# Kernel tuning notes

Hardware: AMD Instinct MI355X
Metric: run time of the kernel (lower is better)

## Reference

```python
import jax, jax.numpy as jnp
import numpy as np

B, N, D, K = 16, 1024, 512, 32
EPS = 1e-12  # F.normalize default eps


def setup_inputs() -> dict:
    key = jax.random.key(0)
    k1, k2, k3 = jax.random.split(key, 3)
    x = jax.random.normal(k1, (B, N, D), dtype=jnp.float32)
    mask = (jax.random.uniform(k2, (B, N)) < 0.9).astype(jnp.float32)
    centroids = jax.random.uniform(k3, (D, K), dtype=jnp.float32)
    # _init_params: conv.weight = 2*alpha*centroids, conv.bias = -alpha*||centroids||_col
    W = 2.0 * centroids
    b = -jnp.linalg.norm(centroids, axis=0)
    return {"x": x, "mask": mask, "W": W, "b": b, "centroids": centroids}


def reference(x, mask, W, b, centroids):
    # descriptor-wise L2 normalization (normalize_input=True)
    xn = x / jnp.maximum(jnp.linalg.norm(x, axis=2, keepdims=True), EPS)
    # 1x1 conv (matmul) + bias, masked logits
    logits = (jnp.einsum('bnd,dk->bnk', xn, W) + b) * mask[:, :, None]
    soft_assign = jax.nn.softmax(logits, axis=2) * mask[:, :, None]  # (B,N,K)
    # entropy with -log2(0) -> 0 (matches log_p[isinf]=0 since sa*0 = 0 there)
    safe = jnp.where(soft_assign > 0, soft_assign, 1.0)
    assign_entropy = -(soft_assign * jnp.log2(safe)).sum() / mask.sum()
    # cluster-usage distribution
    assign_sum = soft_assign.sum(axis=1)  # (B,K)
    assign_dist = jax.nn.log_softmax(assign_sum, axis=1)
    # NetVLAD residual pooling, algebraically fused (avoids (B,N,D,K) tensor):
    # vlad[b,d,k] = sum_n xn*sa - centroids[d,k]*sum_n sa
    vlad = jnp.einsum('bnd,bnk->bdk', xn, soft_assign) - centroids[None] * assign_sum[:, None, :]
    vlad = vlad / jnp.maximum(jnp.linalg.norm(vlad, axis=1, keepdims=True), EPS)
    vlad = jnp.transpose(vlad, (0, 2, 1))  # (B,K,D)
    return (vlad, assign_dist, assign_entropy)
```

## Files before the change

kernel.cpp:

```cpp
#include <hip/hip_runtime.h>
#include <math.h>

#define B 16
#define N 1024
#define D 512
#define K 32
#define EPSF 1e-12f

#define WS_CT_F   0
#define WS_ASP_F  16384
#define WS_ENTP_F 49152
#define WS_MSKP_F 50176
#define WS_PART_F 51200

#define OFF_DIST 262144
#define OFF_ENT  262656

typedef __attribute__((ext_vector_type(8))) short s16x8;
typedef __attribute__((ext_vector_type(4))) short s16x4;
typedef __attribute__((ext_vector_type(4))) float f32x4;

__device__ __forceinline__ ushort f2b(float f) {
    unsigned u = __builtin_bit_cast(unsigned, f);
    u += 0x7fffu + ((u >> 16) & 1u);
    return (ushort)(u >> 16);
}
__device__ __forceinline__ float b2f(ushort u) {
    return __builtin_bit_cast(float, (unsigned)u << 16);
}

struct SH {
    union U {
        ushort wtl[32 * 512];
        struct Q {
            ushort xs[4 * 2048];
            ushort xsT[512 * 36];
        } q;
    } u;
    ushort tls[32 * 32];
    float4 accsh[2 * 128];
    float ssqsh[32], invsh[32];
};

__global__ __launch_bounds__(256, 2) void kA2(const float* __restrict__ x,
    const float* __restrict__ mask, const float* __restrict__ Wf,
    const float* __restrict__ bias, const float* __restrict__ cent,
    float* __restrict__ ws, ushort* __restrict__ parts)
{
    __shared__ SH sh;
    const int bid = blockIdx.x;
    const int b = bid >> 4;
    const int s64 = bid & 15;
    const int tid = threadIdx.x;
    const int w = tid >> 6;
    const int rw = w & 1, dw = w >> 1;
    const int l = tid & 63;
    const int g = l >> 4, lo = l & 15;

    if (tid < 64) {
        int k = tid & 31, dd = tid >> 5;
        int d = bid * 2 + dd;
        ws[WS_CT_F + k * 512 + d] = cent[d * 32 + k];
    }
    {
        const float4* Wg = (const float4*)Wf;
        #pragma unroll
        for (int i = 0; i < 16; ++i) {
            int f4 = tid + i * 256;
            float4 v = Wg[f4];
            int d = f4 >> 3, k4 = (f4 & 7) << 2;
            float vv[4] = {v.x, v.y, v.z, v.w};
            #pragma unroll
            for (int j = 0; j < 4; ++j) {
                int k = k4 + j;
                sh.u.wtl[(k * 512 + d) ^ ((k & 7) << 3)] = f2b(vv[j]);
            }
        }
    }
    __syncthreads();
    s16x8 afr0[2][4], afr1[2][4];
    #pragma unroll
    for (int cc = 0; cc < 2; ++cc)
        #pragma unroll
        for (int ks = 0; ks < 4; ++ks) {
            int dglob = (dw * 2 + cc) * 128 + ks * 32 + g * 8;
            afr0[cc][ks] = *(const s16x8*)&sh.u.wtl[(lo * 512 + dglob) ^ ((lo & 7) << 3)];
            afr1[cc][ks] = *(const s16x8*)&sh.u.wtl[((16 + lo) * 512 + dglob) ^ ((lo & 7) << 3)];
        }
    __syncthreads();

    ushort* xw = sh.u.q.xs + w * 2048;
    ushort* xsT = sh.u.q.xsT;

    f32x4 acc2[2][8];
    #pragma unroll
    for (int kt = 0; kt < 2; ++kt)
        #pragma unroll
        for (int dt = 0; dt < 8; ++dt)
            acc2[kt][dt] = (f32x4){0.f, 0.f, 0.f, 0.f};

    #pragma unroll
    for (int tile = 0; tile < 2; ++tile) {
        const int n0 = s64 * 64 + tile * 32 + rw * 16;
        const int p = bid * 4 + tile * 2 + rw;

        float ssq[8] = {0.f, 0.f, 0.f, 0.f, 0.f, 0.f, 0.f, 0.f};
        f32x4 acc[2] = {{0.f, 0.f, 0.f, 0.f}, {0.f, 0.f, 0.f, 0.f}};
        const float4* xg = (const float4*)(x + (size_t)(b * N + n0) * D);

        #pragma unroll
        for (int cc = 0; cc < 2; ++cc) {
            const int c = dw * 2 + cc;
            float4 fv[8];
            #pragma unroll
            for (int j = 0; j < 8; ++j) {
                int idx = l + 64 * j;
                fv[j] = xg[(idx >> 5) * 128 + c * 32 + (idx & 31)];
            }
            #pragma unroll
            for (int j = 0; j < 8; ++j)
                ssq[j] += fv[j].x * fv[j].x + fv[j].y * fv[j].y
                        + fv[j].z * fv[j].z + fv[j].w * fv[j].w;
            #pragma unroll
            for (int j = 0; j < 8; ++j) {
                int idx = l + 64 * j;
                int r = idx >> 5, c4 = idx & 31;
                unsigned bo = (unsigned)(c4 * 8) ^ (unsigned)((r & 7) << 4);
                s16x4 sv = { (short)f2b(fv[j].x), (short)f2b(fv[j].y),
                             (short)f2b(fv[j].z), (short)f2b(fv[j].w) };
                *(s16x4*)&xw[r * 128 + (bo >> 1)] = sv;
                int nn = rw * 16 + r;
                int dbase = c * 128 + c4 * 4;
                xsT[(dbase + 0) * 36 + nn] = (ushort)sv[0];
                xsT[(dbase + 1) * 36 + nn] = (ushort)sv[1];
                xsT[(dbase + 2) * 36 + nn] = (ushort)sv[2];
                xsT[(dbase + 3) * 36 + nn] = (ushort)sv[3];
            }
            #pragma unroll
            for (int ks = 0; ks < 4; ++ks) {
                unsigned bo = (unsigned)(ks * 64 + g * 16) ^ (unsigned)((lo & 7) << 4);
                s16x8 bfrag = *(const s16x8*)&xw[lo * 128 + (bo >> 1)];
                acc[0] = __builtin_amdgcn_mfma_f32_16x16x32_bf16(afr0[cc][ks], bfrag, acc[0], 0, 0, 0);
                acc[1] = __builtin_amdgcn_mfma_f32_16x16x32_bf16(afr1[cc][ks], bfrag, acc[1], 0, 0, 0);
            }
        }

        #pragma unroll
        for (int j = 0; j < 8; ++j) {
            #pragma unroll
            for (int m = 16; m; m >>= 1) ssq[j] += __shfl_xor(ssq[j], m);
        }
        if (dw == 1) {
            if ((l & 31) == 0) {
                #pragma unroll
                for (int j = 0; j < 8; ++j)
                    sh.ssqsh[rw * 16 + (l >> 5) + 2 * j] = ssq[j];
            }
            sh.accsh[rw * 128 + l * 2 + 0] = *(float4*)&acc[0];
            sh.accsh[rw * 128 + l * 2 + 1] = *(float4*)&acc[1];
        }
        __syncthreads();
        if (dw == 0) {
            float4 o0 = sh.accsh[rw * 128 + l * 2 + 0];
            float4 o1 = sh.accsh[rw * 128 + l * 2 + 1];
            acc[0][0] += o0.x; acc[0][1] += o0.y; acc[0][2] += o0.z; acc[0][3] += o0.w;
            acc[1][0] += o1.x; acc[1][1] += o1.y; acc[1][2] += o1.z; acc[1][3] += o1.w;
            if ((l & 31) == 0) {
                #pragma unroll
                for (int j = 0; j < 8; ++j) {
                    int r = (l >> 5) + 2 * j;
                    sh.invsh[rw * 16 + r] = 1.f / fmaxf(sqrtf(ssq[j] + sh.ssqsh[rw * 16 + r]), EPSF);
                }
            }
        }
        __syncthreads();
        if (dw == 0) {
            const float inv = sh.invsh[rw * 16 + lo];
            const float mv = mask[b * N + n0 + lo];
            float lg[2][4];
            #pragma unroll
            for (int kt = 0; kt < 2; ++kt)
                #pragma unroll
                for (int r = 0; r < 4; ++r)
                    lg[kt][r] = (acc[kt][r] * inv + bias[kt * 16 + g * 4 + r]) * mv;
            float mx = lg[0][0];
            #pragma unroll
            for (int kt = 0; kt < 2; ++kt)
                #pragma unroll
                for (int r = 0; r < 4; ++r) mx = fmaxf(mx, lg[kt][r]);
            mx = fmaxf(mx, __shfl_xor(mx, 16));
            mx = fmaxf(mx, __shfl_xor(mx, 32));
            float e[2][4], sum = 0.f;
            #pragma unroll
            for (int kt = 0; kt < 2; ++kt)
                #pragma unroll
                for (int r = 0; r < 4; ++r) { e[kt][r] = __expf(lg[kt][r] - mx); sum += e[kt][r]; }
            sum += __shfl_xor(sum, 16);
            sum += __shfl_xor(sum, 32);
            const float rs = mv / sum;
            float sa[2][4], ent = 0.f;
            #pragma unroll
            for (int kt = 0; kt < 2; ++kt)
                #pragma unroll
                for (int r = 0; r < 4; ++r) {
                    sa[kt][r] = e[kt][r] * rs;
                    ent += sa[kt][r] > 0.f ? -sa[kt][r] * __log2f(sa[kt][r]) : 0.f;
                }
            #pragma unroll
            for (int m = 32; m; m >>= 1) ent += __shfl_xor(ent, m);
            if (l == 0) ws[WS_ENTP_F + p] = ent;
            float mp = mv;
            #pragma unroll
            for (int m = 8; m; m >>= 1) mp += __shfl_xor(mp, m);
            if (l == 0) ws[WS_MSKP_F + p] = mp;
            #pragma unroll
            for (int kt = 0; kt < 2; ++kt)
                #pragma unroll
                for (int r = 0; r < 4; ++r) {
                    float av = sa[kt][r];
                    #pragma unroll
                    for (int m = 8; m; m >>= 1) av += __shfl_xor(av, m);
                    if (lo == 0) ws[WS_ASP_F + p * 32 + kt * 16 + g * 4 + r] = av;
                }
            #pragma unroll
            for (int kt = 0; kt < 2; ++kt)
                #pragma unroll
                for (int r = 0; r < 4; ++r)
                    sh.tls[(kt * 16 + g * 4 + r) * 32 + rw * 16 + lo] = f2b(sa[kt][r] * inv);
        }
        __syncthreads();

        {
            s16x8 av0 = *(const s16x8*)&sh.tls[lo * 32 + g * 8];
            s16x8 av1 = *(const s16x8*)&sh.tls[(16 + lo) * 32 + g * 8];
            #pragma unroll
            for (int dt = 0; dt < 8; ++dt) {
                int d = w * 128 + dt * 16 + lo;
                s16x4 b0 = *(const s16x4*)&xsT[d * 36 + g * 8];
                s16x4 b1 = *(const s16x4*)&xsT[d * 36 + g * 8 + 4];
                s16x8 bv;
                bv[0] = b0[0]; bv[1] = b0[1]; bv[2] = b0[2]; bv[3] = b0[3];
                bv[4] = b1[0]; bv[5] = b1[1]; bv[6] = b1[2]; bv[7] = b1[3];
                acc2[0][dt] = __builtin_amdgcn_mfma_f32_16x16x32_bf16(av0, bv, acc2[0][dt], 0, 0, 0);
                acc2[1][dt] = __builtin_amdgcn_mfma_f32_16x16x32_bf16(av1, bv, acc2[1][dt], 0, 0, 0);
            }
        }
        __syncthreads();
    }

    ushort* stg = sh.u.q.xsT;
    #pragma unroll
    for (int kt = 0; kt < 2; ++kt)
        #pragma unroll
        for (int dt = 0; dt < 8; ++dt)
            #pragma unroll
            for (int r = 0; r < 4; ++r)
                stg[(kt * 16 + g * 4 + r) * 520 + w * 128 + dt * 16 + lo] = f2b(acc2[kt][dt][r]);
    __syncthreads();
    #pragma unroll
    for (int j = 0; j < 8; ++j) {
        int k = w * 8 + j;
        s16x8 v = *(const s16x8*)&stg[k * 520 + l * 8];
        *(s16x8*)(parts + ((size_t)(s64 * 16 + b) * 32 + k) * 512 + l * 8) = v;
    }
}

__global__ __launch_bounds__(256) void kC2(const float* __restrict__ ws,
    const ushort* __restrict__ parts, float* __restrict__ out)
{
    __shared__ float pm[256];
    __shared__ float asL[32];
    __shared__ float red[4];
    const int bid = blockIdx.x;
    const int b = bid >> 5, k = bid & 31;
    const int t = threadIdx.x;
    {
        int kk = t & 31, i = t >> 5;
        float a = 0.f;
        #pragma unroll
        for (int ii = 0; ii < 8; ++ii)
            a += ws[WS_ASP_F + (size_t)(b * 64 + ii * 8 + i) * 32 + kk];
        pm[t] = a;
    }
    __syncthreads();
    if (t < 32) {
        float a = 0.f;
        #pragma unroll
        for (int i = 0; i < 8; ++i) a += pm[i * 32 + t];
        asL[t] = a;
    }
    __syncthreads();
    if (k == 0 && t < 32) {
        float a = asL[t];
        float mx = a;
        #pragma unroll
        for (int m = 16; m; m >>= 1) mx = fmaxf(mx, __shfl_xor(mx, m));
        float e = __expf(a - mx), ssum = e;
        #pragma unroll
        for (int m = 16; m; m >>= 1) ssum += __shfl_xor(ssum, m);
        out[OFF_DIST + b * 32 + t] = a - mx - logf(ssum);
    }
    if (bid == 0 && (t >> 6) == 1) {
        int ll = t & 63;
        float es = 0.f, ms = 0.f;
        for (int i = ll; i < 1024; i += 64) {
            es += ws[WS_ENTP_F + i];
            ms += ws[WS_MSKP_F + i];
        }
        #pragma unroll
        for (int m = 32; m; m >>= 1) { es += __shfl_xor(es, m); ms += __shfl_xor(ms, m); }
        if (ll == 0) out[OFF_ENT] = es / ms;
    }
    const float as = asL[k];
    const int d0 = t * 2;
    float a0 = 0.f, a1 = 0.f;
    #pragma unroll
    for (int s = 0; s < 16; ++s) {
        unsigned v = *(const unsigned*)(parts + ((size_t)(s * 16 + b) * 32 + k) * 512 + d0);
        a0 += b2f((ushort)(v & 0xffffu));
        a1 += b2f((ushort)(v >> 16));
    }
    float2 ctv = *(const float2*)(ws + WS_CT_F + (size_t)k * 512 + d0);
    float v0 = a0 - ctv.x * as;
    float v1 = a1 - ctv.y * as;
    float sq = v0 * v0 + v1 * v1;
    #pragma unroll
    for (int m = 32; m; m >>= 1) sq += __shfl_xor(sq, m);
    if ((t & 63) == 0) red[t >> 6] = sq;
    __syncthreads();
    float sc = 1.f / fmaxf(sqrtf(red[0] + red[1] + red[2] + red[3]), EPSF);
    float2 o = make_float2(v0 * sc, v1 * sc);
    *(float2*)(out + (size_t)(b * 32 + k) * 512 + d0) = o;
}

extern "C" void kernel_launch(void* const* d_in, const int* in_sizes, int n_in,
                              void* d_out, int out_size, void* d_ws, size_t ws_size,
                              hipStream_t stream)
{
    const float* x    = (const float*)d_in[0];
    const float* mask = (const float*)d_in[1];
    const float* W    = (const float*)d_in[2];
    const float* bias = (const float*)d_in[3];
    const float* cent = (const float*)d_in[4];
    float* out = (float*)d_out;
    float* ws  = (float*)d_ws;
    ushort* parts = (ushort*)(ws + WS_PART_F);

    kA2<<<dim3(256), dim3(256), 0, stream>>>(x, mask, W, bias, cent, ws, parts);
    kC2<<<dim3(512), dim3(256), 0, stream>>>(ws, parts, out);
}
```

Baseline: 30.15 us.

## Fuse finalize kernel into main kernel via per-batch atomic counters

Merges the two-kernel pipeline into one kernel. Each block bumps a per-batch arrival counter, spins until all 16 blocks of its batch have arrived, and then finalizes two clusters of that batch: it reduces the partials, subtracts the centroid term and normalizes. The centroid transpose into the workspace is dropped, the W load pattern is reordered, and the transposed shared-memory stores are rotated to reduce bank conflicts. This removes a kernel launch and its gap, but adds a memset launch, spin-waits that assume all blocks are co-resident, and uncoalesced centroid reads.

```diff
diff --git a/kernel.cpp b/kernel.cpp
--- a/kernel.cpp
+++ b/kernel.cpp
@@ -7,11 +7,11 @@
 #define K 32
 #define EPSF 1e-12f
 
-#define WS_CT_F   0
-#define WS_ASP_F  16384
-#define WS_ENTP_F 49152
-#define WS_MSKP_F 50176
-#define WS_PART_F 51200
+#define WS_ASP_F  0
+#define WS_ENTP_F 32768
+#define WS_MSKP_F 33792
+#define WS_CNT_F  34816
+#define WS_PART_F 34880
 
 #define OFF_DIST 262144
 #define OFF_ENT  262656
@@ -42,10 +42,10 @@
     float ssqsh[32], invsh[32];
 };
 
-__global__ __launch_bounds__(256, 2) void kA2(const float* __restrict__ x,
+__global__ __launch_bounds__(256, 2) void kF(const float* __restrict__ x,
     const float* __restrict__ mask, const float* __restrict__ Wf,
     const float* __restrict__ bias, const float* __restrict__ cent,
-    float* __restrict__ ws, ushort* __restrict__ parts)
+    float* __restrict__ ws, ushort* __restrict__ parts, float* __restrict__ out)
 {
     __shared__ SH sh;
     const int bid = blockIdx.x;
@@ -56,23 +56,19 @@
     const int rw = w & 1, dw = w >> 1;
     const int l = tid & 63;
     const int g = l >> 4, lo = l & 15;
-
-    if (tid < 64) {
-        int k = tid & 31, dd = tid >> 5;
-        int d = bid * 2 + dd;
-        ws[WS_CT_F + k * 512 + d] = cent[d * 32 + k];
-    }
+    int* cnt = (int*)(ws + WS_CNT_F);
+
     {
         const float4* Wg = (const float4*)Wf;
         #pragma unroll
         for (int i = 0; i < 16; ++i) {
-            int f4 = tid + i * 256;
-            float4 v = Wg[f4];
-            int d = f4 >> 3, k4 = (f4 & 7) << 2;
+            int d = tid * 2 + (i >> 3);
+            int kq = i & 7;
+            float4 v = Wg[d * 8 + kq];
             float vv[4] = {v.x, v.y, v.z, v.w};
             #pragma unroll
             for (int j = 0; j < 4; ++j) {
-                int k = k4 + j;
+                int k = kq * 4 + j;
                 sh.u.wtl[(k * 512 + d) ^ ((k & 7) << 3)] = f2b(vv[j]);
             }
         }
@@ -131,10 +127,11 @@
                 *(s16x4*)&xw[r * 128 + (bo >> 1)] = sv;
                 int nn = rw * 16 + r;
                 int dbase = c * 128 + c4 * 4;
-                xsT[(dbase + 0) * 36 + nn] = (ushort)sv[0];
-                xsT[(dbase + 1) * 36 + nn] = (ushort)sv[1];
-                xsT[(dbase + 2) * 36 + nn] = (ushort)sv[2];
-                xsT[(dbase + 3) * 36 + nn] = (ushort)sv[3];
+                #pragma unroll
+                for (int m = 0; m < 4; ++m) {
+                    int jj = (m + c4) & 3;
+                    xsT[(dbase + jj) * 36 + nn] = (ushort)sv[jj];
+                }
             }
             #pragma unroll
             for (int ks = 0; ks < 4; ++ks) {
@@ -263,74 +260,95 @@
         s16x8 v = *(const s16x8*)&stg[k * 520 + l * 8];
         *(s16x8*)(parts + ((size_t)(s64 * 16 + b) * 32 + k) * 512 + l * 8) = v;
     }
-}
-
-__global__ __launch_bounds__(256) void kC2(const float* __restrict__ ws,
-    const ushort* __restrict__ parts, float* __restrict__ out)
-{
-    __shared__ float pm[256];
-    __shared__ float asL[32];
-    __shared__ float red[4];
-    const int bid = blockIdx.x;
-    const int b = bid >> 5, k = bid & 31;
-    const int t = threadIdx.x;
+
+    __syncthreads();
+    if (tid == 0) {
+        __threadfence();
+        atomicAdd(&cnt[b], 1);
+        atomicAdd(&cnt[16], 1);
+    }
+
+    const int bF = b;
+    if (tid == 0) {
+        while (__hip_atomic_load(&cnt[bF], __ATOMIC_RELAXED, __HIP_MEMORY_SCOPE_AGENT) < 16)
+            __builtin_amdgcn_s_sleep(8);
+        __threadfence();
+    }
+    __syncthreads();
+
+    float* pmB = (float*)sh.accsh;
     {
-        int kk = t & 31, i = t >> 5;
+        int kk = tid & 31, ii = tid >> 5;
         float a = 0.f;
         #pragma unroll
-        for (int ii = 0; ii < 8; ++ii)
-            a += ws[WS_ASP_F + (size_t)(b * 64 + ii * 8 + i) * 32 + kk];
-        pm[t] = a;
-    }
-    __syncthreads();
-    if (t < 32) {
+        for (int jj = 0; jj < 8; ++jj)
+            a += ws[WS_ASP_F + (size_t)(bF * 64 + jj * 8 + ii) * 32 + kk];
+        pmB[tid] = a;
+    }
+    __syncthreads();
+    if (tid < 32) {
         float a = 0.f;
         #pragma unroll
-        for (int i = 0; i < 8; ++i) a += pm[i * 32 + t];
-        asL[t] = a;
-    }
-    __syncthreads();
-    if (k == 0 && t < 32) {
-        float a = asL[t];
-        float mx = a;
-        #pragma unroll
-        for (int m = 16; m; m >>= 1) mx = fmaxf(mx, __shfl_xor(mx, m));
-        float e = __expf(a - mx), ssum = e;
-        #pragma unroll
-        for (int m = 16; m; m >>= 1) ssum += __shfl_xor(ssum, m);
-        out[OFF_DIST + b * 32 + t] = a - mx - logf(ssum);
-    }
-    if (bid == 0 && (t >> 6) == 1) {
-        int ll = t & 63;
-        float es = 0.f, ms = 0.f;
-        for (int i = ll; i < 1024; i += 64) {
-            es += ws[WS_ENTP_F + i];
-            ms += ws[WS_MSKP_F + i];
-        }
-        #pragma unroll
-        for (int m = 32; m; m >>= 1) { es += __shfl_xor(es, m); ms += __shfl_xor(ms, m); }
-        if (ll == 0) out[OFF_ENT] = es / ms;
-    }
-    const float as = asL[k];
-    const int d0 = t * 2;
-    float a0 = 0.f, a1 = 0.f;
-    #pragma unroll
-    for (int s = 0; s < 16; ++s) {
-        unsigned v = *(const unsigned*)(parts + ((size_t)(s * 16 + b) * 32 + k) * 512 + d0);
-        a0 += b2f((ushort)(v & 0xffffu));
-        a1 += b2f((ushort)(v >> 16));
-    }
-    float2 ctv = *(const float2*)(ws + WS_CT_F + (size_t)k * 512 + d0);
-    float v0 = a0 - ctv.x * as;
-    float v1 = a1 - ctv.y * as;
-    float sq = v0 * v0 + v1 * v1;
-    #pragma unroll
-    for (int m = 32; m; m >>= 1) sq += __shfl_xor(sq, m);
-    if ((t & 63) == 0) red[t >> 6] = sq;
-    __syncthreads();
-    float sc = 1.f / fmaxf(sqrtf(red[0] + red[1] + red[2] + red[3]), EPSF);
-    float2 o = make_float2(v0 * sc, v1 * sc);
-    *(float2*)(out + (size_t)(b * 32 + k) * 512 + d0) = o;
+        for (int i2 = 0; i2 < 8; ++i2) a += pmB[i2 * 32 + tid];
+        sh.ssqsh[tid] = a;
+        if ((bid & 15) == 0) {
+            float mx = a;
+            #pragma unroll
+            for (int m = 16; m; m >>= 1) mx = fmaxf(mx, __shfl_xor(mx, m));
+            float e = __expf(a - mx), ssum = e;
+            #pragma unroll
+            for (int m = 16; m; m >>= 1) ssum += __shfl_xor(ssum, m);
+            out[OFF_DIST + bF * 32 + tid] = a - mx - logf(ssum);
+        }
+    }
+    __syncthreads();
+
+    const int k0 = (bid * 2) & 31;
+    #pragma unroll
+    for (int q = 0; q < 2; ++q) {
+        const int k = k0 + q;
+        const float as = sh.ssqsh[k];
+        const int d0 = tid * 2;
+        float a0 = 0.f, a1 = 0.f;
+        #pragma unroll
+        for (int s2 = 0; s2 < 16; ++s2) {
+            unsigned v = *(const unsigned*)(parts + ((size_t)(s2 * 16 + bF) * 32 + k) * 512 + d0);
+            a0 += b2f((ushort)(v & 0xffffu));
+            a1 += b2f((ushort)(v >> 16));
+        }
+        float c0 = cent[(size_t)d0 * 32 + k];
+        float c1 = cent[(size_t)(d0 + 1) * 32 + k];
+        float v0 = a0 - c0 * as;
+        float v1 = a1 - c1 * as;
+        float sq = v0 * v0 + v1 * v1;
+        #pragma unroll
+        for (int m = 32; m; m >>= 1) sq += __shfl_xor(sq, m);
+        if ((tid & 63) == 0) sh.invsh[tid >> 6] = sq;
+        __syncthreads();
+        float sc = 1.f / fmaxf(sqrtf(sh.invsh[0] + sh.invsh[1] + sh.invsh[2] + sh.invsh[3]), EPSF);
+        float2 o = make_float2(v0 * sc, v1 * sc);
+        *(float2*)(out + (size_t)(bF * 32 + k) * 512 + d0) = o;
+        __syncthreads();
+    }
+
+    if (bid == 0) {
+        if (tid == 0) {
+            while (__hip_atomic_load(&cnt[16], __ATOMIC_RELAXED, __HIP_MEMORY_SCOPE_AGENT) < 256)
+                __builtin_amdgcn_s_sleep(8);
+            __threadfence();
+        }
+        __syncthreads();
+        if (tid < 64) {
+            float es = 0.f, ms = 0.f;
+            for (int i = tid; i < 1024; i += 64) {
+                es += ws[WS_ENTP_F + i];
+                ms += ws[WS_MSKP_F + i];
+            }
+            #pragma unroll
+            for (int m = 32; m; m >>= 1) { es += __shfl_xor(es, m); ms += __shfl_xor(ms, m); }
+            if (tid == 0) out[OFF_ENT] = es / ms;
+        }
+    }
 }
 
 extern "C" void kernel_launch(void* const* d_in, const int* in_sizes, int n_in,
@@ -346,6 +364,6 @@
     float* ws  = (float*)d_ws;
     ushort* parts = (ushort*)(ws + WS_PART_F);
 
-    kA2<<<dim3(256), dim3(256), 0, stream>>>(x, mask, W, bias, cent, ws, parts);
-    kC2<<<dim3(512), dim3(256), 0, stream>>>(ws, parts, out);
+    hipMemsetAsync((void*)(ws + WS_CNT_F), 0, 128, stream);
+    kF<<<dim3(256), dim3(256), 0, stream>>>(x, mask, W, bias, cent, ws, parts, out);
 }
```

Result: slower. 63.00 us (+108.9%).

## Double block to 512 threads splitting D across four waves per row group

Applied to the files above, without the earlier changes.

The first kernel now launches 512 threads per block, so each wave handles one 128-wide D chunk instead of two. The cross-wave reduction of logits and squared norms now goes through shared memory over four partial sums. The transposed x tile is built with lane shuffles and byte permutes into packed 16-byte stores, using an XOR swizzle in place of the padded layout. The aim is more memory-level parallelism and fewer scattered 2-byte LDS writes, at the cost of a larger reduction, more barriers and more shared memory per block.

```diff
diff --git a/kernel.cpp b/kernel.cpp
--- a/kernel.cpp
+++ b/kernel.cpp
@@ -19,6 +19,7 @@
 typedef __attribute__((ext_vector_type(8))) short s16x8;
 typedef __attribute__((ext_vector_type(4))) short s16x4;
 typedef __attribute__((ext_vector_type(4))) float f32x4;
+typedef __attribute__((ext_vector_type(4))) unsigned u32x4;
 
 __device__ __forceinline__ ushort f2b(float f) {
     unsigned u = __builtin_bit_cast(unsigned, f);
@@ -33,16 +34,19 @@
     union U {
         ushort wtl[32 * 512];
         struct Q {
-            ushort xs[4 * 2048];
-            ushort xsT[512 * 36];
+            union {
+                ushort xs[8 * 2048];
+                float4 accsh[1024];
+            };
+            ushort xsT[512 * 32];
         } q;
     } u;
     ushort tls[32 * 32];
-    float4 accsh[2 * 128];
-    float ssqsh[32], invsh[32];
+    float ssqsh[4][32];
+    float invsh[32];
 };
 
-__global__ __launch_bounds__(256, 2) void kA2(const float* __restrict__ x,
+__global__ __launch_bounds__(512, 2) void kA3(const float* __restrict__ x,
     const float* __restrict__ mask, const float* __restrict__ Wf,
     const float* __restrict__ bias, const float* __restrict__ cent,
     float* __restrict__ ws, ushort* __restrict__ parts)
@@ -52,8 +56,8 @@
     const int b = bid >> 4;
     const int s64 = bid & 15;
     const int tid = threadIdx.x;
-    const int w = tid >> 6;
-    const int rw = w & 1, dw = w >> 1;
+    const int w_ = tid >> 6;
+    const int rw = w_ & 1, dw = w_ >> 1;
     const int l = tid & 63;
     const int g = l >> 4, lo = l & 15;
 
@@ -65,38 +69,37 @@
     {
         const float4* Wg = (const float4*)Wf;
         #pragma unroll
-        for (int i = 0; i < 16; ++i) {
-            int f4 = tid + i * 256;
+        for (int i = 0; i < 8; ++i) {
+            int f4 = tid + i * 512;
             float4 v = Wg[f4];
-            int d = f4 >> 3, k4 = (f4 & 7) << 2;
+            int d = f4 >> 3, kq = (f4 & 7) << 2;
             float vv[4] = {v.x, v.y, v.z, v.w};
             #pragma unroll
             for (int j = 0; j < 4; ++j) {
-                int k = k4 + j;
+                int k = kq + j;
                 sh.u.wtl[(k * 512 + d) ^ ((k & 7) << 3)] = f2b(vv[j]);
             }
         }
     }
     __syncthreads();
-    s16x8 afr0[2][4], afr1[2][4];
-    #pragma unroll
-    for (int cc = 0; cc < 2; ++cc)
-        #pragma unroll
-        for (int ks = 0; ks < 4; ++ks) {
-            int dglob = (dw * 2 + cc) * 128 + ks * 32 + g * 8;
-            afr0[cc][ks] = *(const s16x8*)&sh.u.wtl[(lo * 512 + dglob) ^ ((lo & 7) << 3)];
-            afr1[cc][ks] = *(const s16x8*)&sh.u.wtl[((16 + lo) * 512 + dglob) ^ ((lo & 7) << 3)];
-        }
-    __syncthreads();
-
-    ushort* xw = sh.u.q.xs + w * 2048;
+    s16x8 afr0[4], afr1[4];
+    #pragma unroll
+    for (int ks = 0; ks < 4; ++ks) {
+        int dglob = dw * 128 + ks * 32 + g * 8;
+        afr0[ks] = *(const s16x8*)&sh.u.wtl[(lo * 512 + dglob) ^ ((lo & 7) << 3)];
+        afr1[ks] = *(const s16x8*)&sh.u.wtl[((16 + lo) * 512 + dglob) ^ ((lo & 7) << 3)];
+    }
+    __syncthreads();
+
+    ushort* xw = sh.u.q.xs + w_ * 2048;
     ushort* xsT = sh.u.q.xsT;
-
-    f32x4 acc2[2][8];
+    float4* accsh = sh.u.q.accsh;
+
+    f32x4 acc2[2][4];
     #pragma unroll
     for (int kt = 0; kt < 2; ++kt)
         #pragma unroll
-        for (int dt = 0; dt < 8; ++dt)
+        for (int dt = 0; dt < 4; ++dt)
             acc2[kt][dt] = (f32x4){0.f, 0.f, 0.f, 0.f};
 
     #pragma unroll
@@ -104,72 +107,94 @@
         const int n0 = s64 * 64 + tile * 32 + rw * 16;
         const int p = bid * 4 + tile * 2 + rw;
 
-        float ssq[8] = {0.f, 0.f, 0.f, 0.f, 0.f, 0.f, 0.f, 0.f};
         f32x4 acc[2] = {{0.f, 0.f, 0.f, 0.f}, {0.f, 0.f, 0.f, 0.f}};
         const float4* xg = (const float4*)(x + (size_t)(b * N + n0) * D);
 
-        #pragma unroll
-        for (int cc = 0; cc < 2; ++cc) {
-            const int c = dw * 2 + cc;
-            float4 fv[8];
+        float4 fv[8];
+        #pragma unroll
+        for (int j = 0; j < 8; ++j) {
+            int idx = l + 64 * j;
+            fv[j] = xg[(idx >> 5) * 128 + dw * 32 + (idx & 31)];
+        }
+        float ssq[8];
+        #pragma unroll
+        for (int j = 0; j < 8; ++j)
+            ssq[j] = fv[j].x * fv[j].x + fv[j].y * fv[j].y
+                   + fv[j].z * fv[j].z + fv[j].w * fv[j].w;
+        unsigned b01[8], b23[8];
+        #pragma unroll
+        for (int j = 0; j < 8; ++j) {
+            b01[j] = (unsigned)f2b(fv[j].x) | ((unsigned)f2b(fv[j].y) << 16);
+            b23[j] = (unsigned)f2b(fv[j].z) | ((unsigned)f2b(fv[j].w) << 16);
+        }
+        #pragma unroll
+        for (int j = 0; j < 8; ++j) {
+            int r = 2 * j + (l >> 5);
+            int c4 = l & 31;
+            unsigned bo = (unsigned)(c4 * 8) ^ (unsigned)((r & 7) << 4);
+            *(uint2*)&xw[r * 128 + (bo >> 1)] = make_uint2(b01[j], b23[j]);
+        }
+        {
+            unsigned oth[8];
             #pragma unroll
             for (int j = 0; j < 8; ++j) {
-                int idx = l + 64 * j;
-                fv[j] = xg[(idx >> 5) * 128 + c * 32 + (idx & 31)];
-            }
+                unsigned sel = (l < 32) ? b23[j] : b01[j];
+                oth[j] = (unsigned)__shfl_xor((int)sel, 32);
+            }
+            unsigned w0[8], w1[8];
+            #pragma unroll
+            for (int j = 0; j < 8; ++j) {
+                unsigned a = (l < 32) ? b01[j] : oth[j];
+                unsigned bb = (l < 32) ? oth[j] : b23[j];
+                w0[j] = __byte_perm(a, bb, 0x5410);
+                w1[j] = __byte_perm(a, bb, 0x7632);
+            }
+            const int d0 = dw * 128 + (l & 31) * 4 + ((l >> 5) << 1);
+            const int s_ = l & 3;
+            const int c0 = (2 * rw) ^ s_, c1 = (2 * rw + 1) ^ s_;
+            *(u32x4*)&xsT[d0 * 32 + c0 * 8]       = (u32x4){w0[0], w0[1], w0[2], w0[3]};
+            *(u32x4*)&xsT[d0 * 32 + c1 * 8]       = (u32x4){w0[4], w0[5], w0[6], w0[7]};
+            *(u32x4*)&xsT[(d0 + 1) * 32 + c0 * 8] = (u32x4){w1[0], w1[1], w1[2], w1[3]};
+            *(u32x4*)&xsT[(d0 + 1) * 32 + c1 * 8] = (u32x4){w1[4], w1[5], w1[6], w1[7]};
+        }
+        #pragma unroll
+        for (int ks = 0; ks < 4; ++ks) {
+            unsigned bo = (unsigned)(ks * 64 + g * 16) ^ (unsigned)((lo & 7) << 4);
+            s16x8 bfrag = *(const s16x8*)&xw[lo * 128 + (bo >> 1)];
+            acc[0] = __builtin_amdgcn_mfma_f32_16x16x32_bf16(afr0[ks], bfrag, acc[0], 0, 0, 0);
+            acc[1] = __builtin_amdgcn_mfma_f32_16x16x32_bf16(afr1[ks], bfrag, acc[1], 0, 0, 0);
+        }
+        #pragma unroll
+        for (int j = 0; j < 8; ++j) {
+            #pragma unroll
+            for (int m = 16; m; m >>= 1) ssq[j] += __shfl_xor(ssq[j], m);
+        }
+        __syncthreads();
+        accsh[dw * 256 + rw * 128 + l * 2 + 0] = *(float4*)&acc[0];
+        accsh[dw * 256 + rw * 128 + l * 2 + 1] = *(float4*)&acc[1];
+        if ((l & 31) == 0) {
             #pragma unroll
             for (int j = 0; j < 8; ++j)
-                ssq[j] += fv[j].x * fv[j].x + fv[j].y * fv[j].y
-                        + fv[j].z * fv[j].z + fv[j].w * fv[j].w;
-            #pragma unroll
-            for (int j = 0; j < 8; ++j) {
-                int idx = l + 64 * j;
-                int r = idx >> 5, c4 = idx & 31;
-                unsigned bo = (unsigned)(c4 * 8) ^ (unsigned)((r & 7) << 4);
-                s16x4 sv = { (short)f2b(fv[j].x), (short)f2b(fv[j].y),
-                             (short)f2b(fv[j].z), (short)f2b(fv[j].w) };
-                *(s16x4*)&xw[r * 128 + (bo >> 1)] = sv;
-                int nn = rw * 16 + r;
-                int dbase = c * 128 + c4 * 4;
-                xsT[(dbase + 0) * 36 + nn] = (ushort)sv[0];
-                xsT[(dbase + 1) * 36 + nn] = (ushort)sv[1];
-                xsT[(dbase + 2) * 36 + nn] = (ushort)sv[2];
-                xsT[(dbase + 3) * 36 + nn] = (ushort)sv[3];
-            }
-            #pragma unroll
-            for (int ks = 0; ks < 4; ++ks) {
-                unsigned bo = (unsigned)(ks * 64 + g * 16) ^ (unsigned)((lo & 7) << 4);
-                s16x8 bfrag = *(const s16x8*)&xw[lo * 128 + (bo >> 1)];
-                acc[0] = __builtin_amdgcn_mfma_f32_16x16x32_bf16(afr0[cc][ks], bfrag, acc[0], 0, 0, 0);
-                acc[1] = __builtin_amdgcn_mfma_f32_16x16x32_bf16(afr1[cc][ks], bfrag, acc[1], 0, 0, 0);
-            }
-        }
-
-        #pragma unroll
-        for (int j = 0; j < 8; ++j) {
-            #pragma unroll
-            for (int m = 16; m; m >>= 1) ssq[j] += __shfl_xor(ssq[j], m);
-        }
-        if (dw == 1) {
+                sh.ssqsh[dw][rw * 16 + 2 * j + (l >> 5)] = ssq[j];
+        }
+        __syncthreads();
+        if (dw == 0) {
+            f32x4 a0 = {0.f,0.f,0.f,0.f}, a1 = {0.f,0.f,0.f,0.f};
+            #pragma unroll
+            for (int q = 0; q < 4; ++q) {
+                float4 v0 = accsh[q * 256 + rw * 128 + l * 2 + 0];
+                float4 v1 = accsh[q * 256 + rw * 128 + l * 2 + 1];
+                a0[0] += v0.x; a0[1] += v0.y; a0[2] += v0.z; a0[3] += v0.w;
+                a1[0] += v1.x; a1[1] += v1.y; a1[2] += v1.z; a1[3] += v1.w;
+            }
+            acc[0] = a0; acc[1] = a1;
             if ((l & 31) == 0) {
                 #pragma unroll
-                for (int j = 0; j < 8; ++j)
-                    sh.ssqsh[rw * 16 + (l >> 5) + 2 * j] = ssq[j];
-            }
-            sh.accsh[rw * 128 + l * 2 + 0] = *(float4*)&acc[0];
-            sh.accsh[rw * 128 + l * 2 + 1] = *(float4*)&acc[1];
-        }
-        __syncthreads();
-        if (dw == 0) {
-            float4 o0 = sh.accsh[rw * 128 + l * 2 + 0];
-            float4 o1 = sh.accsh[rw * 128 + l * 2 + 1];
-            acc[0][0] += o0.x; acc[0][1] += o0.y; acc[0][2] += o0.z; acc[0][3] += o0.w;
-            acc[1][0] += o1.x; acc[1][1] += o1.y; acc[1][2] += o1.z; acc[1][3] += o1.w;
-            if ((l & 31) == 0) {
-                #pragma unroll
                 for (int j = 0; j < 8; ++j) {
-                    int r = (l >> 5) + 2 * j;
-                    sh.invsh[rw * 16 + r] = 1.f / fmaxf(sqrtf(ssq[j] + sh.ssqsh[rw * 16 + r]), EPSF);
+                    int r = 2 * j + (l >> 5);
+                    float tot = sh.ssqsh[0][rw * 16 + r] + sh.ssqsh[1][rw * 16 + r]
+                              + sh.ssqsh[2][rw * 16 + r] + sh.ssqsh[3][rw * 16 + r];
+                    sh.invsh[rw * 16 + r] = 1.f / fmaxf(sqrtf(tot), EPSF);
                 }
             }
         }
@@ -233,11 +258,13 @@
         {
             s16x8 av0 = *(const s16x8*)&sh.tls[lo * 32 + g * 8];
             s16x8 av1 = *(const s16x8*)&sh.tls[(16 + lo) * 32 + g * 8];
-            #pragma unroll
-            for (int dt = 0; dt < 8; ++dt) {
-                int d = w * 128 + dt * 16 + lo;
-                s16x4 b0 = *(const s16x4*)&xsT[d * 36 + g * 8];
-                s16x4 b1 = *(const s16x4*)&xsT[d * 36 + g * 8 + 4];
+            const int sr = (lo >> 2) & 3;
+            #pragma unroll
+            for (int dt = 0; dt < 4; ++dt) {
+                int d = w_ * 64 + dt * 16 + lo;
+                const ushort* rp = &xsT[d * 32 + ((g ^ sr)) * 8];
+                s16x4 b0 = *(const s16x4*)rp;
+                s16x4 b1 = *(const s16x4*)(rp + 4);
                 s16x8 bv;
                 bv[0] = b0[0]; bv[1] = b0[1]; bv[2] = b0[2]; bv[3] = b0[3];
                 bv[4] = b1[0]; bv[5] = b1[1]; bv[6] = b1[2]; bv[7] = b1[3];
@@ -248,20 +275,22 @@
         __syncthreads();
     }
 
-    ushort* stg = sh.u.q.xsT;
+    ushort* stg = (ushort*)&sh.u.q;
     #pragma unroll
     for (int kt = 0; kt < 2; ++kt)
         #pragma unroll
-        for (int dt = 0; dt < 8; ++dt)
+        for (int dt = 0; dt < 4; ++dt)
             #pragma unroll
             for (int r = 0; r < 4; ++r)
-                stg[(kt * 16 + g * 4 + r) * 520 + w * 128 + dt * 16 + lo] = f2b(acc2[kt][dt][r]);
-    __syncthreads();
-    #pragma unroll
-    for (int j = 0; j < 8; ++j) {
-        int k = w * 8 + j;
-        s16x8 v = *(const s16x8*)&stg[k * 520 + l * 8];
-        *(s16x8*)(parts + ((size_t)(s64 * 16 + b) * 32 + k) * 512 + l * 8) = v;
+                stg[(kt * 16 + g * 4 + r) * 520 + w_ * 64 + dt * 16 + lo] = f2b(acc2[kt][dt][r]);
+    __syncthreads();
+    {
+        int k = tid >> 4, m16 = tid & 15;
+        #pragma unroll
+        for (int j = 0; j < 2; ++j) {
+            s16x8 v = *(const s16x8*)&stg[k * 520 + m16 * 32 + j * 16];
+            *(s16x8*)(parts + ((size_t)(s64 * 16 + b) * 32 + k) * 512 + m16 * 32 + j * 16) = v;
+        }
     }
 }
 
@@ -346,6 +375,6 @@
     float* ws  = (float*)d_ws;
     ushort* parts = (ushort*)(ws + WS_PART_F);
 
-    kA2<<<dim3(256), dim3(256), 0, stream>>>(x, mask, W, bias, cent, ws, parts);
+    kA3<<<dim3(256), dim3(512), 0, stream>>>(x, mask, W, bias, cent, ws, parts);
     kC2<<<dim3(512), dim3(256), 0, stream>>>(ws, parts, out);
 }
```

Result: slower. 32.14 us (+6.6%).

## Prefetch second x tile into registers and vectorize swizzled transposed LDS writes

Applied to the files above, without the earlier changes.

Loads the second 32-row x tile into registers while the first tile is being processed, overlapping global loads with compute. Replaces the scalar 2-byte transposed LDS stores with lane-exchange shuffles, byte permutes and 16-byte swizzled stores into an unpadded xsT layout, with a matching XOR-swizzled read. W staging is reindexed so each thread reads contiguous rows. The prefetch holds 32 float4 registers per thread, which raises register pressure under the two-blocks-per-CU launch bound and risks spills.

```diff
diff --git a/kernel.cpp b/kernel.cpp
--- a/kernel.cpp
+++ b/kernel.cpp
@@ -19,6 +19,7 @@
 typedef __attribute__((ext_vector_type(8))) short s16x8;
 typedef __attribute__((ext_vector_type(4))) short s16x4;
 typedef __attribute__((ext_vector_type(4))) float f32x4;
+typedef __attribute__((ext_vector_type(4))) unsigned u32x4;
 
 __device__ __forceinline__ ushort f2b(float f) {
     unsigned u = __builtin_bit_cast(unsigned, f);
@@ -34,7 +35,7 @@
         ushort wtl[32 * 512];
         struct Q {
             ushort xs[4 * 2048];
-            ushort xsT[512 * 36];
+            ushort xsT[512 * 32];
         } q;
     } u;
     ushort tls[32 * 32];
@@ -42,7 +43,7 @@
     float ssqsh[32], invsh[32];
 };
 
-__global__ __launch_bounds__(256, 2) void kA2(const float* __restrict__ x,
+__global__ __launch_bounds__(256, 2) void kA5(const float* __restrict__ x,
     const float* __restrict__ mask, const float* __restrict__ Wf,
     const float* __restrict__ bias, const float* __restrict__ cent,
     float* __restrict__ ws, ushort* __restrict__ parts)
@@ -52,8 +53,8 @@
     const int b = bid >> 4;
     const int s64 = bid & 15;
     const int tid = threadIdx.x;
-    const int w = tid >> 6;
-    const int rw = w & 1, dw = w >> 1;
+    const int w_ = tid >> 6;
+    const int rw = w_ & 1, dw = w_ >> 1;
     const int l = tid & 63;
     const int g = l >> 4, lo = l & 15;
 
@@ -66,13 +67,13 @@
         const float4* Wg = (const float4*)Wf;
         #pragma unroll
         for (int i = 0; i < 16; ++i) {
-            int f4 = tid + i * 256;
-            float4 v = Wg[f4];
-            int d = f4 >> 3, k4 = (f4 & 7) << 2;
+            int d = tid * 2 + (i >> 3);
+            int kq = i & 7;
+            float4 v = Wg[d * 8 + kq];
             float vv[4] = {v.x, v.y, v.z, v.w};
             #pragma unroll
             for (int j = 0; j < 4; ++j) {
-                int k = k4 + j;
+                int k = kq * 4 + j;
                 sh.u.wtl[(k * 512 + d) ^ ((k & 7) << 3)] = f2b(vv[j]);
             }
         }
@@ -89,7 +90,7 @@
         }
     __syncthreads();
 
-    ushort* xw = sh.u.q.xs + w * 2048;
+    ushort* xw = sh.u.q.xs + w_ * 2048;
     ushort* xsT = sh.u.q.xsT;
 
     f32x4 acc2[2][8];
@@ -98,43 +99,67 @@
         #pragma unroll
         for (int dt = 0; dt < 8; ++dt)
             acc2[kt][dt] = (f32x4){0.f, 0.f, 0.f, 0.f};
+
+    float4 fv[2][16];
+    {
+        const float4* xg = (const float4*)(x + (size_t)(b * N + s64 * 64 + rw * 16) * D);
+        #pragma unroll
+        for (int cc = 0; cc < 2; ++cc)
+            #pragma unroll
+            for (int j = 0; j < 8; ++j) {
+                int idx = l + 64 * j;
+                fv[0][cc * 8 + j] = xg[(idx >> 5) * 128 + (dw * 2 + cc) * 32 + (idx & 31)];
+            }
+    }
 
     #pragma unroll
     for (int tile = 0; tile < 2; ++tile) {
         const int n0 = s64 * 64 + tile * 32 + rw * 16;
         const int p = bid * 4 + tile * 2 + rw;
 
+        f32x4 acc[2] = {{0.f, 0.f, 0.f, 0.f}, {0.f, 0.f, 0.f, 0.f}};
         float ssq[8] = {0.f, 0.f, 0.f, 0.f, 0.f, 0.f, 0.f, 0.f};
-        f32x4 acc[2] = {{0.f, 0.f, 0.f, 0.f}, {0.f, 0.f, 0.f, 0.f}};
-        const float4* xg = (const float4*)(x + (size_t)(b * N + n0) * D);
 
         #pragma unroll
         for (int cc = 0; cc < 2; ++cc) {
             const int c = dw * 2 + cc;
-            float4 fv[8];
+            unsigned b01[8], b23[8];
             #pragma unroll
             for (int j = 0; j < 8; ++j) {
-                int idx = l + 64 * j;
-                fv[j] = xg[(idx >> 5) * 128 + c * 32 + (idx & 31)];
-            }
-            #pragma unroll
-            for (int j = 0; j < 8; ++j)
-                ssq[j] += fv[j].x * fv[j].x + fv[j].y * fv[j].y
-                        + fv[j].z * fv[j].z + fv[j].w * fv[j].w;
+                float4 f = fv[tile][cc * 8 + j];
+                ssq[j] += f.x * f.x + f.y * f.y + f.z * f.z + f.w * f.w;
+                b01[j] = (unsigned)f2b(f.x) | ((unsigned)f2b(f.y) << 16);
+                b23[j] = (unsigned)f2b(f.z) | ((unsigned)f2b(f.w) << 16);
+            }
             #pragma unroll
             for (int j = 0; j < 8; ++j) {
-                int idx = l + 64 * j;
-                int r = idx >> 5, c4 = idx & 31;
+                int r = 2 * j + (l >> 5);
+                int c4 = l & 31;
                 unsigned bo = (unsigned)(c4 * 8) ^ (unsigned)((r & 7) << 4);
-                s16x4 sv = { (short)f2b(fv[j].x), (short)f2b(fv[j].y),
-                             (short)f2b(fv[j].z), (short)f2b(fv[j].w) };
-                *(s16x4*)&xw[r * 128 + (bo >> 1)] = sv;
-                int nn = rw * 16 + r;
-                int dbase = c * 128 + c4 * 4;
-                xsT[(dbase + 0) * 36 + nn] = (ushort)sv[0];
-                xsT[(dbase + 1) * 36 + nn] = (ushort)sv[1];
-                xsT[(dbase + 2) * 36 + nn] = (ushort)sv[2];
-                xsT[(dbase + 3) * 36 + nn] = (ushort)sv[3];
+                *(uint2*)&xw[r * 128 + (bo >> 1)] = make_uint2(b01[j], b23[j]);
+            }
+            {
+                unsigned oth[8];
+                #pragma unroll
+                for (int j = 0; j < 8; ++j) {
+                    unsigned sel = (l < 32) ? b23[j] : b01[j];
+                    oth[j] = (unsigned)__shfl_xor((int)sel, 32);
+                }
+                unsigned w0[8], w1[8];
+                #pragma unroll
+                for (int j = 0; j < 8; ++j) {
+                    unsigned a = (l < 32) ? b01[j] : oth[j];
+                    unsigned bb = (l < 32) ? oth[j] : b23[j];
+                    w0[j] = __byte_perm(a, bb, 0x5410);
+                    w1[j] = __byte_perm(a, bb, 0x7632);
+                }
+                const int d0 = c * 128 + (l & 31) * 4 + ((l >> 5) << 1);
+                const int s_ = l & 3;
+                const int c0 = (2 * rw) ^ s_, c1 = (2 * rw + 1) ^ s_;
+                *(u32x4*)&xsT[d0 * 32 + c0 * 8]       = (u32x4){w0[0], w0[1], w0[2], w0[3]};
+                *(u32x4*)&xsT[d0 * 32 + c1 * 8]       = (u32x4){w0[4], w0[5], w0[6], w0[7]};
+                *(u32x4*)&xsT[(d0 + 1) * 32 + c0 * 8] = (u32x4){w1[0], w1[1], w1[2], w1[3]};
+                *(u32x4*)&xsT[(d0 + 1) * 32 + c1 * 8] = (u32x4){w1[4], w1[5], w1[6], w1[7]};
             }
             #pragma unroll
             for (int ks = 0; ks < 4; ++ks) {
@@ -143,6 +168,17 @@
                 acc[0] = __builtin_amdgcn_mfma_f32_16x16x32_bf16(afr0[cc][ks], bfrag, acc[0], 0, 0, 0);
                 acc[1] = __builtin_amdgcn_mfma_f32_16x16x32_bf16(afr1[cc][ks], bfrag, acc[1], 0, 0, 0);
             }
+        }
+
+        if (tile == 0) {
+            const float4* xg = (const float4*)(x + (size_t)(b * N + s64 * 64 + 32 + rw * 16) * D);
+            #pragma unroll
+            for (int cc = 0; cc < 2; ++cc)
+                #pragma unroll
+                for (int j = 0; j < 8; ++j) {
+                    int idx = l + 64 * j;
+                    fv[1][cc * 8 + j] = xg[(idx >> 5) * 128 + (dw * 2 + cc) * 32 + (idx & 31)];
+                }
         }
 
         #pragma unroll
@@ -233,11 +269,13 @@
         {
             s16x8 av0 = *(const s16x8*)&sh.tls[lo * 32 + g * 8];
             s16x8 av1 = *(const s16x8*)&sh.tls[(16 + lo) * 32 + g * 8];
+            const int sr = (lo >> 2) & 3;
             #pragma unroll
             for (int dt = 0; dt < 8; ++dt) {
-                int d = w * 128 + dt * 16 + lo;
-                s16x4 b0 = *(const s16x4*)&xsT[d * 36 + g * 8];
-                s16x4 b1 = *(const s16x4*)&xsT[d * 36 + g * 8 + 4];
+                int d = w_ * 128 + dt * 16 + lo;
+                const ushort* rp = &xsT[d * 32 + (g ^ sr) * 8];
+                s16x4 b0 = *(const s16x4*)rp;
+                s16x4 b1 = *(const s16x4*)(rp + 4);
                 s16x8 bv;
                 bv[0] = b0[0]; bv[1] = b0[1]; bv[2] = b0[2]; bv[3] = b0[3];
                 bv[4] = b1[0]; bv[5] = b1[1]; bv[6] = b1[2]; bv[7] = b1[3];
@@ -248,18 +286,18 @@
         __syncthreads();
     }
 
-    ushort* stg = sh.u.q.xsT;
+    ushort* stg = (ushort*)&sh.u.q;
     #pragma unroll
     for (int kt = 0; kt < 2; ++kt)
         #pragma unroll
         for (int dt = 0; dt < 8; ++dt)
             #pragma unroll
             for (int r = 0; r < 4; ++r)
-                stg[(kt * 16 + g * 4 + r) * 520 + w * 128 + dt * 16 + lo] = f2b(acc2[kt][dt][r]);
+                stg[(kt * 16 + g * 4 + r) * 520 + w_ * 128 + dt * 16 + lo] = f2b(acc2[kt][dt][r]);
     __syncthreads();
     #pragma unroll
     for (int j = 0; j < 8; ++j) {
-        int k = w * 8 + j;
+        int k = w_ * 8 + j;
         s16x8 v = *(const s16x8*)&stg[k * 520 + l * 8];
         *(s16x8*)(parts + ((size_t)(s64 * 16 + b) * 32 + k) * 512 + l * 8) = v;
     }
@@ -346,6 +384,6 @@
     float* ws  = (float*)d_ws;
     ushort* parts = (ushort*)(ws + WS_PART_F);
 
-    kA2<<<dim3(256), dim3(256), 0, stream>>>(x, mask, W, bias, cent, ws, parts);
+    kA5<<<dim3(256), dim3(256), 0, stream>>>(x, mask, W, bias, cent, ws, parts);
     kC2<<<dim3(512), dim3(256), 0, stream>>>(ws, parts, out);
 }
```

Measured after the change: 31.82 us. 5.5% more time.
